# Performance work log

Hardware: AMD Instinct MI355X
Metric: run time of the kernel (lower is better)

Reference implementation:

```python
import jax, jax.numpy as jnp
import numpy as np

DEGREE = 3        # self.degree = 3 in MGNN
K = 3             # Chebyshev/polynomial order of the GCN
BANDWIDTH = 512.0 # Gaussian kernel bandwidth (~2*d so adj spans (0,1])
B, N, D_IN = 2, 4096, 256
D_OUT = 64        # 2*D_OUT == 128 == linear output dim


def _bspline(t, degree):
    """Cox-de Boor recursive B-spline basis N_{0,degree}(t), elementwise,
    uniform knots on [0,1]. t: [B,N,N] adjacency values."""
    knots = np.linspace(0.0, 1.0, degree + 2)  # static python floats
    basis = [jnp.where((t >= knots[i]) & (t < knots[i + 1]), 1.0, 0.0).astype(t.dtype)
             for i in range(degree + 1)]
    for k in range(1, degree + 1):
        basis = [
            (t - knots[i]) / (knots[i + k] - knots[i]) * basis[i]
            + (knots[i + k + 1] - t) / (knots[i + k + 1] - knots[i + 1]) * basis[i + 1]
            for i in range(degree + 1 - k)
        ]
    return basis[0]


def _wavelet(t, degree):
    # spline wavelet: difference of dilated/shifted B-splines
    return _bspline(2.0 * t, degree) - _bspline(2.0 * t - 1.0, degree)


def _graph_construction(x, bandwidth):
    # Gaussian-kernel dense adjacency per batch element: [B,N,N], values in (0,1]
    sq = jnp.sum(x * x, axis=-1)                                   # [B,N]
    d2 = sq[:, :, None] + sq[:, None, :] - 2.0 * jnp.einsum('bnd,bmd->bnm', x, x)
    d2 = jnp.maximum(d2, 0.0)
    return jnp.exp(-d2 / bandwidth)


def _gcn(x, kernel, Wk):
    # out = sum_k (kernel^k x) W_k ; Wk: [K, D_IN, D_OUT]
    h = x
    out = jnp.einsum('bnd,do->bno', h, Wk[0])
    for k in range(1, Wk.shape[0]):
        h = jnp.einsum('bnm,bmd->bnd', kernel, h)
        out = out + jnp.einsum('bnd,do->bno', h, Wk[k])
    return out


def setup_inputs() -> dict:
    key = jax.random.key(0)
    k0, k1, k2, k3 = jax.random.split(key, 4)
    x = jax.random.normal(k0, (B, N, D_IN), dtype=jnp.float32)
    Wk = jax.random.normal(k1, (K, D_IN, D_OUT), dtype=jnp.float32) * 0.05
    W_lin = jax.random.normal(k2, (D_IN, 2 * D_OUT), dtype=jnp.float32) * 0.05
    b_lin = jnp.zeros((2 * D_OUT,), dtype=jnp.float32)
    return {"x": x, "Wk": Wk, "W_lin": W_lin, "b_lin": b_lin}


def reference(x, Wk, W_lin, b_lin):
    adj = _graph_construction(x, BANDWIDTH)       # [B,N,N]
    b_kernel = _bspline(adj, DEGREE)              # [B,N,N]
    w_kernel = _wavelet(adj, DEGREE)              # [B,N,N]
    gcn1 = _gcn(x, b_kernel, Wk)                  # [B,N,D_OUT]
    gcn2 = _gcn(x, w_kernel, Wk)                  # [B,N,D_OUT]
    akgcn = jnp.concatenate([gcn1, gcn2], axis=-1)        # [B,N,2*D_OUT]
    akgcn = jax.nn.relu(akgcn + x @ W_lin + b_lin)        # residual + relu
    return akgcn.reshape(akgcn.shape[0], -1)              # flatten last two dims
```

## Files before the change

### kernel.cpp

```cpp
#include <hip/hip_runtime.h>
#include <hip/hip_bf16.h>

typedef __hip_bfloat16 bf16;
typedef float v4f __attribute__((ext_vector_type(4)));
typedef short v8s __attribute__((ext_vector_type(8)));

typedef const __attribute__((address_space(1))) void gvoid;
typedef __attribute__((address_space(3))) void lvoid;

__device__ __forceinline__ void async16(const void* g, void* l) {
  __builtin_amdgcn_global_load_lds((gvoid*)g, (lvoid*)l, 16, 0, 0);
}

__device__ __forceinline__ unsigned short f2bf(float v) {
  __hip_bfloat16 h = __float2bfloat16(v);
  return *(unsigned short*)&h;
}
__device__ __forceinline__ float bflo(unsigned dw) {
  unsigned u = dw << 16;
  return *(float*)&u;
}
__device__ __forceinline__ float bfhi(unsigned dw) {
  unsigned u = dw & 0xffff0000u;
  return *(float*)&u;
}

__device__ __forceinline__ float b3(float u) {
  u = fminf(fmaxf(u, 0.f), 4.f);
  float t1 = fmaxf(u - 1.f, 0.f);
  float t2 = fmaxf(u - 2.f, 0.f);
  float t3 = fmaxf(u - 3.f, 0.f);
  float c0 = u * u * u;
  float c1 = t1 * t1 * t1;
  float c2 = t2 * t2 * t2;
  float c3 = t3 * t3 * t3;
  return (c0 - 4.f * c1 + 6.f * c2 - 4.f * c3) * (1.f / 6.f);
}

template <int NI, int BK>
__device__ __forceinline__ void mfma_loop(const bf16* __restrict__ A,
                                          const bf16* __restrict__ B, int lda,
                                          int ldb, int kLen, bf16* As, bf16* Bs,
                                          v4f acc[4][NI]) {
  const int tid = threadIdx.x;
  const int wave = tid >> 6;
  const int lane = tid & 63;
  const int quad = lane >> 4;
  const int r16 = lane & 15;
  const int wm = (wave >> 1) * 64;
  const int wn = (wave & 1) * (NI * 16);
  constexpr int CPR = BK / 8;
  constexpr int AQ = 128 * CPR / 256;
  constexpr int BQ = NI * 32 * CPR / 256;
  char* AsC = (char*)As;
  char* BsC = (char*)Bs;
  for (int kk = 0; kk < kLen; kk += BK) {
#pragma unroll
    for (int q = 0; q < AQ; ++q) {
      const int ch = tid + 256 * q;
      const int r = ch / CPR, c = (ch % CPR) * 8;
      async16(A + (size_t)r * lda + kk + c, AsC + q * 4096 + wave * 1024);
    }
#pragma unroll
    for (int q = 0; q < BQ; ++q) {
      const int ch = tid + 256 * q;
      const int r = ch / CPR, c = (ch % CPR) * 8;
      async16(B + (size_t)r * ldb + kk + c, BsC + q * 4096 + wave * 1024);
    }
    __syncthreads();
#pragma unroll
    for (int ks = 0; ks < BK / 32; ++ks) {
      v8s af[4], bfr[NI];
#pragma unroll
      for (int mi = 0; mi < 4; ++mi)
        af[mi] =
            *(const v8s*)(As + (wm + mi * 16 + r16) * BK + ks * 32 + quad * 8);
#pragma unroll
      for (int ni = 0; ni < NI; ++ni)
        bfr[ni] =
            *(const v8s*)(Bs + (wn + ni * 16 + r16) * BK + ks * 32 + quad * 8);
#pragma unroll
      for (int mi = 0; mi < 4; ++mi)
#pragma unroll
        for (int ni = 0; ni < NI; ++ni)
          acc[mi][ni] = __builtin_amdgcn_mfma_f32_16x16x32_bf16(
              af[mi], bfr[ni], acc[mi][ni], 0, 0, 0);
    }
    __syncthreads();
  }
}

__global__ void prep(const float* __restrict__ x, bf16* __restrict__ U,
                     float* __restrict__ sq) {
  const int n = blockIdx.x, b = blockIdx.y, t = threadIdx.x;
  const size_t row = (size_t)b * 4096 + n;
  float v = x[row * 256 + t];
  U[row * 1280 + t] = __float2bfloat16(v);
  float s = v * v;
#pragma unroll
  for (int o = 32; o > 0; o >>= 1) s += __shfl_down(s, o, 64);
  __shared__ float ls[4];
  if ((t & 63) == 0) ls[t >> 6] = s;
  __syncthreads();
  if (t == 0) sq[row] = ls[0] + ls[1] + ls[2] + ls[3];
}

__global__ void transk(const float* __restrict__ src, bf16* __restrict__ dst) {
  __shared__ float tile[64][65];
  const int z = blockIdx.z;
  const float* s = src + (size_t)z * 4096 * 256;
  bf16* d = dst + (size_t)z * 256 * 4096;
  const int n0 = blockIdx.x * 64, d0 = blockIdx.y * 64;
  const int tx = threadIdx.x & 31, ty = threadIdx.x >> 5;
#pragma unroll
  for (int i = 0; i < 8; ++i) {
    const int r = ty + i * 8;
    const float2 v = *(const float2*)(s + (size_t)(n0 + r) * 256 + d0 + tx * 2);
    tile[r][tx * 2] = v.x;
    tile[r][tx * 2 + 1] = v.y;
  }
  __syncthreads();
#pragma unroll
  for (int i = 0; i < 8; ++i) {
    const int c = ty + i * 8;
    __hip_bfloat162 p;
    p.x = __float2bfloat16(tile[tx * 2][c]);
    p.y = __float2bfloat16(tile[tx * 2 + 1][c]);
    *(__hip_bfloat162*)(d + (size_t)(d0 + c) * 4096 + n0 + tx * 2) = p;
  }
}

__global__ void wbig(const float* __restrict__ Wk, const float* __restrict__ Wl,
                     bf16* __restrict__ WbT) {
  int idx = blockIdx.x * 256 + threadIdx.x;
  if (idx >= 128 * 1280) return;
  int j = idx / 1280, k = idx % 1280;
  int o = j & 63;
  float v = 0.f;
  if (k < 256)
    v = Wk[k * 64 + o] + Wl[k * 128 + j];
  else if (k < 512)
    v = (j < 64) ? Wk[16384 + (k - 256) * 64 + o] : 0.f;
  else if (k < 768)
    v = (j < 64) ? Wk[32768 + (k - 512) * 64 + o] : 0.f;
  else if (k < 1024)
    v = (j >= 64) ? Wk[16384 + (k - 768) * 64 + o] : 0.f;
  else
    v = (j >= 64) ? Wk[32768 + (k - 1024) * 64 + o] : 0.f;
  WbT[idx] = __float2bfloat16(v);
}

__global__ __launch_bounds__(256, 2) void gemm_s(const bf16* __restrict__ U,
                                                 const float* __restrict__ sq,
                                                 bf16* __restrict__ kmat) {
  __shared__ __align__(16) bf16 As[128 * 64];
  __shared__ __align__(16) bf16 Bs[128 * 64];
  __shared__ unsigned lut[2048];
  const int tid = threadIdx.x;
  for (int i = tid; i < 2048; i += 256) {
    float t = (i + 0.5f) * (1.f / 2048.f);
    float bv = b3(4.f * t);
    float wv = b3(8.f * t) - b3(8.f * t - 4.f);
    lut[i] = (unsigned)f2bf(bv) | ((unsigned)f2bf(wv) << 16);
  }
  const int z = blockIdx.z;
  const bf16* A = U + (size_t)z * 4096 * 1280 + (size_t)blockIdx.x * 128 * 1280;
  const bf16* B = U + (size_t)z * 4096 * 1280 + (size_t)blockIdx.y * 128 * 1280;
  v4f acc[4][4];
#pragma unroll
  for (int a = 0; a < 4; ++a)
#pragma unroll
    for (int b2 = 0; b2 < 4; ++b2) acc[a][b2] = (v4f){0.f, 0.f, 0.f, 0.f};
  mfma_loop<4, 64>(A, B, 1280, 1280, 256, As, Bs, acc);
  const int wave = tid >> 6, lane = tid & 63;
  const int quad = lane >> 4, r16 = lane & 15;
  const int wm = (wave >> 1) * 64, wn = (wave & 1) * 64;
  const float* sqr = sq + (size_t)z * 4096;
  unsigned short* bk = (unsigned short*)(kmat + (size_t)(z * 2) * 4096 * 4096);
  unsigned short* wk = bk + (size_t)4096 * 4096;
  const int i0 = blockIdx.x * 128 + wm + quad * 4;
  const int j0 = blockIdx.y * 128 + wn + r16;
  const int par = lane & 1;
  const int jc = j0 - par;
  float sqj[4];
#pragma unroll
  for (int ni = 0; ni < 4; ++ni) sqj[ni] = sqr[j0 + ni * 16];
  const float c = -1.4426950408889634f / 512.f;
#pragma unroll
  for (int mi = 0; mi < 4; ++mi) {
#pragma unroll
    for (int ni = 0; ni < 4; ++ni) {
      unsigned pv[4];
#pragma unroll
      for (int r = 0; r < 4; ++r) {
        float s = acc[mi][ni][r];
        float d2 = fmaxf(sqr[i0 + mi * 16 + r] + sqj[ni] - 2.f * s, 0.f);
        float t = __builtin_amdgcn_exp2f(d2 * c);
        int idx = (int)fminf(t * 2048.f, 2047.f);
        pv[r] = lut[idx];
      }
      unsigned ov[4];
#pragma unroll
      for (int r = 0; r < 4; ++r) ov[r] = __shfl_xor((int)pv[r], 1, 64);
#pragma unroll
      for (int rr = 0; rr < 2; ++rr) {
        const int r = par * 2 + rr;
        const unsigned a = pv[r], b2 = ov[r];
        const unsigned lo = par ? b2 : a;
        const unsigned hi = par ? a : b2;
        const unsigned bkd = (lo & 0xffffu) | (hi << 16);
        const unsigned wkd = (lo >> 16) | (hi & 0xffff0000u);
        const int i = i0 + mi * 16 + r;
        const size_t off = (size_t)i * 4096 + jc + ni * 16;
        *(unsigned*)(bk + off) = bkd;
        *(unsigned*)(wk + off) = wkd;
      }
    }
  }
}

__global__ __launch_bounds__(512, 2) void gemm_h(const bf16* __restrict__ kmat,
                                                 const bf16* __restrict__ BtBase,
                                                 bf16* __restrict__ hpart,
                                                 int btShift) {
  __shared__ __align__(16) bf16 As[128 * 64];
  __shared__ __align__(16) bf16 Bs[256 * 64];
  const int bz = blockIdx.z;
  const int z = bz >> 2, split = bz & 3;
  const int kk0 = split * 1024;
  const bf16* A =
      kmat + (size_t)z * 4096 * 4096 + (size_t)blockIdx.x * 128 * 4096 + kk0;
  const bf16* B = BtBase + (size_t)(z >> btShift) * 256 * 4096 + kk0;
  const int tid = threadIdx.x, wave = tid >> 6, lane = tid & 63;
  const int quad = lane >> 4, r16 = lane & 15;
  const int wm = (wave >> 2) * 64;
  const int wn = (wave & 3) * 64;
  char* AsC = (char*)As;
  char* BsC = (char*)Bs;
  v4f acc[4][4];
#pragma unroll
  for (int a = 0; a < 4; ++a)
#pragma unroll
    for (int b2 = 0; b2 < 4; ++b2) acc[a][b2] = (v4f){0.f, 0.f, 0.f, 0.f};
  for (int kk = 0; kk < 1024; kk += 64) {
#pragma unroll
    for (int q = 0; q < 2; ++q) {
      const int ch = tid + 512 * q;
      const int r = ch >> 3, c = (ch & 7) * 8;
      async16(A + (size_t)r * 4096 + kk + c, AsC + q * 8192 + wave * 1024);
    }
#pragma unroll
    for (int q = 0; q < 4; ++q) {
      const int ch = tid + 512 * q;
      const int r = ch >> 3, c = (ch & 7) * 8;
      async16(B + (size_t)r * 4096 + kk + c, BsC + q * 8192 + wave * 1024);
    }
    __syncthreads();
#pragma unroll
    for (int ks = 0; ks < 2; ++ks) {
      v8s af[4], bfr[4];
#pragma unroll
      for (int mi = 0; mi < 4; ++mi)
        af[mi] =
            *(const v8s*)(As + (wm + mi * 16 + r16) * 64 + ks * 32 + quad * 8);
#pragma unroll
      for (int ni = 0; ni < 4; ++ni)
        bfr[ni] =
            *(const v8s*)(Bs + (wn + ni * 16 + r16) * 64 + ks * 32 + quad * 8);
#pragma unroll
      for (int mi = 0; mi < 4; ++mi)
#pragma unroll
        for (int ni = 0; ni < 4; ++ni)
          acc[mi][ni] = __builtin_amdgcn_mfma_f32_16x16x32_bf16(
              af[mi], bfr[ni], acc[mi][ni], 0, 0, 0);
    }
    __syncthreads();
  }
  bf16* H = hpart + ((size_t)split * 4 + z) * 4096 * 256;
  const int i0 = blockIdx.x * 128 + wm + quad * 4;
  const int j0 = wn + r16;
  const int par = lane & 1;
  const int jc = j0 - par;
#pragma unroll
  for (int mi = 0; mi < 4; ++mi) {
#pragma unroll
    for (int ni = 0; ni < 4; ++ni) {
      unsigned pv[4];
#pragma unroll
      for (int r = 0; r < 4; ++r) pv[r] = (unsigned)f2bf(acc[mi][ni][r]);
      unsigned ov[4];
#pragma unroll
      for (int r = 0; r < 4; ++r) ov[r] = __shfl_xor((int)pv[r], 1, 64);
#pragma unroll
      for (int rr = 0; rr < 2; ++rr) {
        const int r = par * 2 + rr;
        const unsigned a = pv[r], b2 = ov[r];
        const unsigned lo = par ? b2 : a;
        const unsigned hi = par ? a : b2;
        const int i = i0 + mi * 16 + r;
        *(unsigned*)(H + (size_t)i * 256 + jc + ni * 16) = lo | (hi << 16);
      }
    }
  }
}

__global__ void reduceT(const bf16* __restrict__ hpart, bf16* __restrict__ U,
                        bf16* __restrict__ hT, int uoffBase) {
  __shared__ float tile[64][65];
  const int z = blockIdx.z;
  const int b = z >> 1, kern = z & 1;
  const int uoff = uoffBase + kern * 512;
  const int n0 = blockIdx.x * 64, d0 = blockIdx.y * 64;
  const int tx = threadIdx.x & 31, ty = threadIdx.x >> 5;
  const size_t sstride = (size_t)4 * 4096 * 256;
  const bf16* s0 = hpart + (size_t)z * 4096 * 256;
#pragma unroll
  for (int i = 0; i < 8; ++i) {
    const int r = ty + i * 8;
    const size_t off = (size_t)(n0 + r) * 256 + d0 + tx * 2;
    float vx = 0.f, vy = 0.f;
#pragma unroll
    for (int k = 0; k < 4; ++k) {
      const unsigned dw = *(const unsigned*)(s0 + k * sstride + off);
      vx += bflo(dw);
      vy += bfhi(dw);
    }
    tile[r][tx * 2] = vx;
    tile[r][tx * 2 + 1] = vy;
    __hip_bfloat162 p;
    p.x = __float2bfloat16(vx);
    p.y = __float2bfloat16(vy);
    *(__hip_bfloat162*)(U + (size_t)(b * 4096 + n0 + r) * 1280 + uoff + d0 +
                        tx * 2) = p;
  }
  if (hT) {
    __syncthreads();
#pragma unroll
    for (int i = 0; i < 8; ++i) {
      const int c = ty + i * 8;
      __hip_bfloat162 p;
      p.x = __float2bfloat16(tile[tx * 2][c]);
      p.y = __float2bfloat16(tile[tx * 2 + 1][c]);
      *(__hip_bfloat162*)(hT + (size_t)z * 256 * 4096 + (size_t)(d0 + c) * 4096 +
                          n0 + tx * 2) = p;
    }
  }
}

__global__ __launch_bounds__(256, 4) void gemm_proj(
    const bf16* __restrict__ U, const bf16* __restrict__ WbT,
    const float* __restrict__ blin, float* __restrict__ out) {
  __shared__ __align__(16) bf16 As[128 * 64];
  __shared__ __align__(16) bf16 Bs[64 * 64];
  const bf16* A = U + (size_t)blockIdx.x * 128 * 1280;
  const bf16* B = WbT + (size_t)blockIdx.y * 64 * 1280;
  v4f acc[4][2];
#pragma unroll
  for (int a = 0; a < 4; ++a)
#pragma unroll
    for (int b2 = 0; b2 < 2; ++b2) acc[a][b2] = (v4f){0.f, 0.f, 0.f, 0.f};
  mfma_loop<2, 64>(A, B, 1280, 1280, 1280, As, Bs, acc);
  const int tid = threadIdx.x, wave = tid >> 6, lane = tid & 63;
  const int quad = lane >> 4, r16 = lane & 15;
  const int wm = (wave >> 1) * 64, wn = (wave & 1) * 32;
  const int i0 = blockIdx.x * 128 + wm + quad * 4;
  const int j0 = blockIdx.y * 64 + wn + r16;
#pragma unroll
  for (int mi = 0; mi < 4; ++mi)
#pragma unroll
    for (int r = 0; r < 4; ++r) {
      const int i = i0 + mi * 16 + r;
#pragma unroll
      for (int ni = 0; ni < 2; ++ni) {
        const int j = j0 + ni * 16;
        out[(size_t)i * 128 + j] = fmaxf(acc[mi][ni][r] + blin[j], 0.f);
      }
    }
}

extern "C" void kernel_launch(void* const* d_in, const int* in_sizes, int n_in,
                              void* d_out, int out_size, void* d_ws,
                              size_t ws_size, hipStream_t stream) {
  const float* x = (const float*)d_in[0];
  const float* Wk = (const float*)d_in[1];
  const float* Wlin = (const float*)d_in[2];
  const float* blin = (const float*)d_in[3];
  float* out = (float*)d_out;
  char* w = (char*)d_ws;
  bf16* kmat = (bf16*)(w);
  bf16* hpart = (bf16*)(w + 134217728);
  bf16* h1T = (bf16*)(w + 201326592);
  bf16* xhT = (bf16*)(w + 209715200);
  bf16* U = (bf16*)(w + 213909504);
  bf16* WbT = (bf16*)(w + 234881024);
  float* sqv = (float*)(w + 235208704);

  prep<<<dim3(4096, 2), 256, 0, stream>>>(x, U, sqv);
  transk<<<dim3(64, 4, 2), 256, 0, stream>>>(x, xhT);
  wbig<<<dim3(640), 256, 0, stream>>>(Wk, Wlin, WbT);
  gemm_s<<<dim3(32, 32, 2), 256, 0, stream>>>(U, sqv, kmat);
  gemm_h<<<dim3(32, 1, 16), 512, 0, stream>>>(kmat, xhT, hpart, 1);
  reduceT<<<dim3(64, 4, 4), 256, 0, stream>>>(hpart, U, h1T, 256);
  gemm_h<<<dim3(32, 1, 16), 512, 0, stream>>>(kmat, h1T, hpart, 0);
  reduceT<<<dim3(64, 4, 4), 256, 0, stream>>>(hpart, U, nullptr, 512);
  gemm_proj<<<dim3(64, 2), 256, 0, stream>>>(U, WbT, blin, out);
}
```

Measured before the change: 248.5 us.

## Drop split-K in propagation GEMM and fuse reduction/transpose epilogue

The propagation GEMM no longer splits K four ways. Each 256-thread block now covers 32 rows across the full 4096-long K dimension and writes bf16 results straight into U and, when needed, a transposed copy for the next hop. This removes the separate reduceT kernels, the partial-sum buffer, and two launches. The cost is a much smaller M tile (32 instead of 128), so B-operand reuse per block drops and each block's loop runs four times longer, with 512 blocks in the grid.

```diff
diff --git a/kernel.cpp b/kernel.cpp
--- a/kernel.cpp
+++ b/kernel.cpp
@@ -15,14 +15,6 @@
 __device__ __forceinline__ unsigned short f2bf(float v) {
   __hip_bfloat16 h = __float2bfloat16(v);
   return *(unsigned short*)&h;
-}
-__device__ __forceinline__ float bflo(unsigned dw) {
-  unsigned u = dw << 16;
-  return *(float*)&u;
-}
-__device__ __forceinline__ float bfhi(unsigned dw) {
-  unsigned u = dw & 0xffff0000u;
-  return *(float*)&u;
 }
 
 __device__ __forceinline__ float b3(float u) {
@@ -219,56 +211,55 @@
   }
 }
 
-__global__ __launch_bounds__(512, 2) void gemm_h(const bf16* __restrict__ kmat,
+__global__ __launch_bounds__(256, 2) void gemm_h(const bf16* __restrict__ kmat,
                                                  const bf16* __restrict__ BtBase,
-                                                 bf16* __restrict__ hpart,
-                                                 int btShift) {
-  __shared__ __align__(16) bf16 As[128 * 64];
+                                                 bf16* __restrict__ U,
+                                                 bf16* __restrict__ hT,
+                                                 int btShift, int uoffBase) {
+  __shared__ __align__(16) bf16 As[32 * 64];
   __shared__ __align__(16) bf16 Bs[256 * 64];
-  const int bz = blockIdx.z;
-  const int z = bz >> 2, split = bz & 3;
-  const int kk0 = split * 1024;
-  const bf16* A =
-      kmat + (size_t)z * 4096 * 4096 + (size_t)blockIdx.x * 128 * 4096 + kk0;
-  const bf16* B = BtBase + (size_t)(z >> btShift) * 256 * 4096 + kk0;
+  __shared__ __align__(16) unsigned short tile[32][264];
+  const int z = blockIdx.z;
+  const int b = z >> 1, kern = z & 1;
+  const int uoff = uoffBase + kern * 512;
+  const int n0 = blockIdx.x * 32;
+  const bf16* A = kmat + (size_t)z * 4096 * 4096 + (size_t)n0 * 4096;
+  const bf16* B = BtBase + (size_t)(z >> btShift) * 256 * 4096;
   const int tid = threadIdx.x, wave = tid >> 6, lane = tid & 63;
   const int quad = lane >> 4, r16 = lane & 15;
-  const int wm = (wave >> 2) * 64;
-  const int wn = (wave & 3) * 64;
+  const int wn = wave * 64;
   char* AsC = (char*)As;
   char* BsC = (char*)Bs;
-  v4f acc[4][4];
-#pragma unroll
-  for (int a = 0; a < 4; ++a)
+  v4f acc[2][4];
+#pragma unroll
+  for (int a = 0; a < 2; ++a)
 #pragma unroll
     for (int b2 = 0; b2 < 4; ++b2) acc[a][b2] = (v4f){0.f, 0.f, 0.f, 0.f};
-  for (int kk = 0; kk < 1024; kk += 64) {
-#pragma unroll
-    for (int q = 0; q < 2; ++q) {
-      const int ch = tid + 512 * q;
+  for (int kk = 0; kk < 4096; kk += 64) {
+    {
+      const int r = tid >> 3, c = (tid & 7) * 8;
+      async16(A + (size_t)r * 4096 + kk + c, AsC + wave * 1024);
+    }
+#pragma unroll
+    for (int q = 0; q < 8; ++q) {
+      const int ch = tid + 256 * q;
       const int r = ch >> 3, c = (ch & 7) * 8;
-      async16(A + (size_t)r * 4096 + kk + c, AsC + q * 8192 + wave * 1024);
-    }
-#pragma unroll
-    for (int q = 0; q < 4; ++q) {
-      const int ch = tid + 512 * q;
-      const int r = ch >> 3, c = (ch & 7) * 8;
-      async16(B + (size_t)r * 4096 + kk + c, BsC + q * 8192 + wave * 1024);
+      async16(B + (size_t)r * 4096 + kk + c, BsC + q * 4096 + wave * 1024);
     }
     __syncthreads();
 #pragma unroll
     for (int ks = 0; ks < 2; ++ks) {
-      v8s af[4], bfr[4];
-#pragma unroll
-      for (int mi = 0; mi < 4; ++mi)
+      v8s af[2], bfr[4];
+#pragma unroll
+      for (int mi = 0; mi < 2; ++mi)
         af[mi] =
-            *(const v8s*)(As + (wm + mi * 16 + r16) * 64 + ks * 32 + quad * 8);
+            *(const v8s*)(As + (mi * 16 + r16) * 64 + ks * 32 + quad * 8);
 #pragma unroll
       for (int ni = 0; ni < 4; ++ni)
         bfr[ni] =
             *(const v8s*)(Bs + (wn + ni * 16 + r16) * 64 + ks * 32 + quad * 8);
 #pragma unroll
-      for (int mi = 0; mi < 4; ++mi)
+      for (int mi = 0; mi < 2; ++mi)
 #pragma unroll
         for (int ni = 0; ni < 4; ++ni)
           acc[mi][ni] = __builtin_amdgcn_mfma_f32_16x16x32_bf16(
@@ -276,74 +267,31 @@
     }
     __syncthreads();
   }
-  bf16* H = hpart + ((size_t)split * 4 + z) * 4096 * 256;
-  const int i0 = blockIdx.x * 128 + wm + quad * 4;
-  const int j0 = wn + r16;
-  const int par = lane & 1;
-  const int jc = j0 - par;
-#pragma unroll
-  for (int mi = 0; mi < 4; ++mi) {
-#pragma unroll
-    for (int ni = 0; ni < 4; ++ni) {
-      unsigned pv[4];
-#pragma unroll
-      for (int r = 0; r < 4; ++r) pv[r] = (unsigned)f2bf(acc[mi][ni][r]);
-      unsigned ov[4];
-#pragma unroll
-      for (int r = 0; r < 4; ++r) ov[r] = __shfl_xor((int)pv[r], 1, 64);
-#pragma unroll
-      for (int rr = 0; rr < 2; ++rr) {
-        const int r = par * 2 + rr;
-        const unsigned a = pv[r], b2 = ov[r];
-        const unsigned lo = par ? b2 : a;
-        const unsigned hi = par ? a : b2;
-        const int i = i0 + mi * 16 + r;
-        *(unsigned*)(H + (size_t)i * 256 + jc + ni * 16) = lo | (hi << 16);
-      }
-    }
-  }
-}
-
-__global__ void reduceT(const bf16* __restrict__ hpart, bf16* __restrict__ U,
-                        bf16* __restrict__ hT, int uoffBase) {
-  __shared__ float tile[64][65];
-  const int z = blockIdx.z;
-  const int b = z >> 1, kern = z & 1;
-  const int uoff = uoffBase + kern * 512;
-  const int n0 = blockIdx.x * 64, d0 = blockIdx.y * 64;
-  const int tx = threadIdx.x & 31, ty = threadIdx.x >> 5;
-  const size_t sstride = (size_t)4 * 4096 * 256;
-  const bf16* s0 = hpart + (size_t)z * 4096 * 256;
-#pragma unroll
-  for (int i = 0; i < 8; ++i) {
-    const int r = ty + i * 8;
-    const size_t off = (size_t)(n0 + r) * 256 + d0 + tx * 2;
-    float vx = 0.f, vy = 0.f;
-#pragma unroll
-    for (int k = 0; k < 4; ++k) {
-      const unsigned dw = *(const unsigned*)(s0 + k * sstride + off);
-      vx += bflo(dw);
-      vy += bfhi(dw);
-    }
-    tile[r][tx * 2] = vx;
-    tile[r][tx * 2 + 1] = vy;
-    __hip_bfloat162 p;
-    p.x = __float2bfloat16(vx);
-    p.y = __float2bfloat16(vy);
-    *(__hip_bfloat162*)(U + (size_t)(b * 4096 + n0 + r) * 1280 + uoff + d0 +
-                        tx * 2) = p;
+#pragma unroll
+  for (int mi = 0; mi < 2; ++mi)
+#pragma unroll
+    for (int ni = 0; ni < 4; ++ni)
+#pragma unroll
+      for (int r = 0; r < 4; ++r)
+        tile[mi * 16 + quad * 4 + r][wn + ni * 16 + r16] =
+            f2bf(acc[mi][ni][r]);
+  __syncthreads();
+  {
+    const int i = tid >> 3, seg = tid & 7;
+    const uint4* src = (const uint4*)&tile[i][seg * 32];
+    uint4* dst =
+        (uint4*)(U + (size_t)(b * 4096 + n0 + i) * 1280 + uoff + seg * 32);
+#pragma unroll
+    for (int q = 0; q < 4; ++q) dst[q] = src[q];
   }
   if (hT) {
-    __syncthreads();
-#pragma unroll
-    for (int i = 0; i < 8; ++i) {
-      const int c = ty + i * 8;
-      __hip_bfloat162 p;
-      p.x = __float2bfloat16(tile[tx * 2][c]);
-      p.y = __float2bfloat16(tile[tx * 2 + 1][c]);
-      *(__hip_bfloat162*)(hT + (size_t)z * 256 * 4096 + (size_t)(d0 + c) * 4096 +
-                          n0 + tx * 2) = p;
-    }
+    const int d = tid;
+    unsigned short tmp[32];
+#pragma unroll
+    for (int i = 0; i < 32; ++i) tmp[i] = tile[i][d];
+    uint4* dst = (uint4*)(hT + (size_t)z * 256 * 4096 + (size_t)d * 4096 + n0);
+#pragma unroll
+    for (int q = 0; q < 4; ++q) dst[q] = ((const uint4*)tmp)[q];
   }
 }
 
@@ -388,20 +336,17 @@
   float* out = (float*)d_out;
   char* w = (char*)d_ws;
   bf16* kmat = (bf16*)(w);
-  bf16* hpart = (bf16*)(w + 134217728);
-  bf16* h1T = (bf16*)(w + 201326592);
-  bf16* xhT = (bf16*)(w + 209715200);
-  bf16* U = (bf16*)(w + 213909504);
-  bf16* WbT = (bf16*)(w + 234881024);
-  float* sqv = (float*)(w + 235208704);
+  bf16* h1T = (bf16*)(w + 134217728);
+  bf16* xhT = (bf16*)(w + 142606336);
+  bf16* U = (bf16*)(w + 146800640);
+  bf16* WbT = (bf16*)(w + 167772160);
+  float* sqv = (float*)(w + 168099840);
 
   prep<<<dim3(4096, 2), 256, 0, stream>>>(x, U, sqv);
   transk<<<dim3(64, 4, 2), 256, 0, stream>>>(x, xhT);
   wbig<<<dim3(640), 256, 0, stream>>>(Wk, Wlin, WbT);
   gemm_s<<<dim3(32, 32, 2), 256, 0, stream>>>(U, sqv, kmat);
-  gemm_h<<<dim3(32, 1, 16), 512, 0, stream>>>(kmat, xhT, hpart, 1);
-  reduceT<<<dim3(64, 4, 4), 256, 0, stream>>>(hpart, U, h1T, 256);
-  gemm_h<<<dim3(32, 1, 16), 512, 0, stream>>>(kmat, h1T, hpart, 0);
-  reduceT<<<dim3(64, 4, 4), 256, 0, stream>>>(hpart, U, nullptr, 512);
+  gemm_h<<<dim3(128, 1, 4), 256, 0, stream>>>(kmat, xhT, U, h1T, 1, 256);
+  gemm_h<<<dim3(128, 1, 4), 256, 0, stream>>>(kmat, h1T, U, nullptr, 0, 512);
   gemm_proj<<<dim3(64, 2), 256, 0, stream>>>(U, WbT, blin, out);
 }
```

Measured after the change: 288.6 us. 16.1% more time.
